# Performance work log

Hardware: AMD Instinct MI355X
Metric: run time of the kernel (lower is better)

## Reference

```python
import jax, jax.numpy as jnp
import numpy as np

IN_FEATURES = [32, 32]
OUT_FEATURES = [64, 64]
RANKS = [16, 16, 16, 16]


def _make_cores(key):
    dims = IN_FEATURES + OUT_FEATURES
    ranks = RANKS
    # init scale as in the torch module
    var = 2 ** (1.0 / len(dims)) / np.prod(np.power(np.array(ranks) + np.array(IN_FEATURES + IN_FEATURES), 1.0 / len(dims)))
    ub = float(np.sqrt(3.0 * var))
    ranks_ext = [ranks[-1]] + list(ranks)
    cores = []
    for i in range(len(dims)):
        key, k = jax.random.split(key)
        cores.append(jax.random.uniform(k, (ranks_ext[i], dims[i], ranks_ext[i + 1]), jnp.float32, -ub, ub))
    return cores, key


def setup_inputs() -> dict:
    key = jax.random.key(0)
    cores, key = _make_cores(key)
    key, kx, kb = jax.random.split(key, 3)
    x = jax.random.normal(kx, (8192, int(np.prod(IN_FEATURES))), jnp.float32)
    bias = jax.random.normal(kb, (int(np.prod(OUT_FEATURES)),), jnp.float32)
    return {"x": x, "core0": cores[0], "core1": cores[1], "core2": cores[2], "core3": cores[3], "bias": bias}


def reference(x, core0, core1, core2, core3, bias):
    # Tensor-ring contraction to build the dense weight, then linear.
    # core shapes: (16,32,16), (16,32,16), (16,64,16), (16,64,16)
    w = jnp.tensordot(core0, core1, axes=([2], [0]))        # (r, i0, i1, r)
    w = jnp.tensordot(w, core2, axes=([3], [0]))            # (r, i0, i1, o0, r)
    # last core: contract w's trailing rank with core axis 0 AND w's leading
    # rank with core's trailing rank (closes the ring) -> (i0, i1, o0, o1)
    w = jnp.tensordot(w, core3, axes=([4, 0], [0, 2]))
    d_out = int(np.prod(OUT_FEATURES))
    w = w.reshape(d_out, -1)                                # (4096, 1024)
    return x @ w.T + bias
```

## Files before the change

### kernel.cpp

```cpp
#include <hip/hip_runtime.h>
#include <hip/hip_bf16.h>
#include <stdint.h>

typedef unsigned short ushort_t;
typedef __attribute__((ext_vector_type(8))) short short8;
typedef __attribute__((ext_vector_type(4))) float floatx4;

__device__ __forceinline__ ushort_t f2bf(float f) {
    union { float f; unsigned u; } v; v.f = f;
    unsigned r = v.u + 0x7fffu + ((v.u >> 16) & 1u);
    return (ushort_t)(r >> 16);
}

__device__ __forceinline__ void async16(ushort_t* lds, const ushort_t* g) {
    __builtin_amdgcn_global_load_lds(
        (const __attribute__((address_space(1))) unsigned int*)g,
        (__attribute__((address_space(3))) unsigned int*)lds, 16, 0, 0);
}

__global__ __launch_bounds__(256) void prep_all(const float* __restrict__ x,
                                                const float* __restrict__ c0,
                                                const float* __restrict__ c1,
                                                const float* __restrict__ c2,
                                                const float* __restrict__ c3,
                                                ushort_t* __restrict__ Xb,
                                                ushort_t* __restrict__ A2b,
                                                ushort_t* __restrict__ Bg1) {
    const int b = blockIdx.x, t = threadIdx.x;
    if (b < 8192) {
        int i = b * 256 + t;
        float4 v = ((const float4*)x)[i];
        ushort4 r;
        r.x = f2bf(v.x); r.y = f2bf(v.y); r.z = f2bf(v.z); r.w = f2bf(v.w);
        ((ushort4*)Xb)[i] = r;
    } else if (b < 9216) {
        int id = (b - 8192) * 256 + t;
        int k = id & 255, ii = id >> 8;
        int r0 = k >> 4, r2 = k & 15;
        int i0 = ii >> 5, i1 = ii & 31;
        const float* p0 = c0 + (r0 * 32 + i0) * 16;
        const float* p1 = c1 + i1 * 16 + r2;
        float s = 0.f;
#pragma unroll
        for (int r1 = 0; r1 < 16; r1++) s += p0[r1] * p1[r1 * 512];
        A2b[id] = f2bf(s);
    } else {
        int id = (b - 9216) * 256 + t;
        int c = id & 1023, n = id >> 10;
        int bq = n >> 8, k = n & 255;
        int r0 = k >> 4, r2 = k & 15;
        int o0 = bq * 16 + (c >> 6), o1 = c & 63;
        const float* p2 = c2 + (r2 * 64 + o0) * 16;
        const float* p3 = c3 + o1 * 16 + r0;
        float s = 0.f;
#pragma unroll
        for (int r3 = 0; r3 < 16; r3++) s += p2[r3] * p3[r3 * 1024];
        Bg1[id] = f2bf(s);
    }
}

__global__ __launch_bounds__(256) void gemm1_u(const ushort_t* __restrict__ Xb,
                                               const ushort_t* __restrict__ Bg1,
                                               ushort_t* __restrict__ U) {
    __shared__ ushort_t As[128 * 32];
    __shared__ ushort_t Bs[128 * 32];
    const int t = threadIdx.x;
    const unsigned orig = blockIdx.x;
    const unsigned wg = (orig & 7) * 64 + (orig >> 3);
    const int row0 = (int)(wg >> 3) * 128;
    const int col0 = (int)(wg & 7) * 128;
    const int w = t >> 6, l = t & 63;
    const int wm = w >> 1, wn = w & 1;
    const int quad = l >> 4, ln = l & 15;

    floatx4 acc[4][4] = {};

    const ushort_t* aSrc = Xb  + (size_t)(row0 + (t >> 2)) * 1024 + (t & 3) * 8;
    const ushort_t* bSrc = Bg1 + (size_t)(col0 + (t >> 2)) * 1024 + (t & 3) * 8;

    for (int kk = 0; kk < 1024; kk += 32) {
        async16(&As[t * 8],        aSrc + kk);
        async16(&As[2048 + t * 8], aSrc + 64 * 1024 + kk);
        async16(&Bs[t * 8],        bSrc + kk);
        async16(&Bs[2048 + t * 8], bSrc + 64 * 1024 + kk);
        __syncthreads();

        short8 a[4], b[4];
#pragma unroll
        for (int ti = 0; ti < 4; ti++)
            a[ti] = *(const short8*)&As[(wm * 64 + ti * 16 + ln) * 32 + quad * 8];
#pragma unroll
        for (int tj = 0; tj < 4; tj++)
            b[tj] = *(const short8*)&Bs[(wn * 64 + tj * 16 + ln) * 32 + quad * 8];
#pragma unroll
        for (int ti = 0; ti < 4; ti++)
#pragma unroll
            for (int tj = 0; tj < 4; tj++)
                acc[ti][tj] = __builtin_amdgcn_mfma_f32_16x16x32_bf16(
                    a[ti], b[tj], acc[ti][tj], 0, 0, 0);
        __syncthreads();
    }

#pragma unroll
    for (int tj = 0; tj < 4; tj++) {
        const int n = col0 + wn * 64 + tj * 16 + ln;
#pragma unroll
        for (int ti = 0; ti < 4; ti++) {
            const int m = row0 + wm * 64 + ti * 16 + quad * 4;
#pragma unroll
            for (int r = 0; r < 4; r++)
                U[(size_t)(m + r) * 1024 + n] = f2bf(acc[ti][tj][r]);
        }
    }
}

__global__ __launch_bounds__(256) void gemm2_tr(const ushort_t* __restrict__ U,
                                                const ushort_t* __restrict__ A2b,
                                                const float* __restrict__ bias,
                                                float* __restrict__ out) {
    __shared__ ushort_t Us[4 * 128 * 32];
    __shared__ ushort_t A2s[32 * 264];
    const int t = threadIdx.x;
    const unsigned orig = blockIdx.x;
    const unsigned wg = (orig & 7) * 256 + (orig >> 3);
    const int jt = (int)(wg & 31), mt = (int)(wg >> 5);
    const int row0 = mt * 128;
    const int a0 = jt * 32;
    const int w = t >> 6, l = t & 63;
    const int wm = w >> 1, wn = w & 1;
    const int quad = l >> 4, ln = l & 15;

    {
        const int r = t >> 3, cb = t & 7;
#pragma unroll
        for (int s = 0; s < 4; s++) {
            int ch = cb + s * 8;
            short8 v = *(const short8*)&A2b[(size_t)(a0 + r) * 256 + ch * 8];
            *(short8*)&A2s[r * 264 + ch * 8] = v;
        }
    }

    floatx4 acc[4][4] = {};

    const ushort_t* uSrc = U + (size_t)(row0 + (t >> 2)) * 1024 + (t & 3) * 8;

    for (int kk = 0; kk < 256; kk += 32) {
#pragma unroll
        for (int b = 0; b < 4; b++) {
            async16(&Us[b * 4096 + t * 8],        uSrc + b * 256 + kk);
            async16(&Us[b * 4096 + 2048 + t * 8], uSrc + 64 * 1024 + b * 256 + kk);
        }
        __syncthreads();

        short8 bfrag = *(const short8*)&A2s[(wn * 16 + ln) * 264 + kk + quad * 8];
#pragma unroll
        for (int b = 0; b < 4; b++) {
            short8 au[4];
#pragma unroll
            for (int ti = 0; ti < 4; ti++)
                au[ti] = *(const short8*)&Us[b * 4096 + (wm * 64 + ti * 16 + ln) * 32 + quad * 8];
#pragma unroll
            for (int ti = 0; ti < 4; ti++)
                acc[b][ti] = __builtin_amdgcn_mfma_f32_16x16x32_bf16(
                    au[ti], bfrag, acc[b][ti], 0, 0, 0);
        }
        __syncthreads();
    }

    const int a = a0 + wn * 16 + ln;
    const float4 bv = ((const float4*)bias)[a];
#pragma unroll
    for (int ti = 0; ti < 4; ti++) {
        const int m = row0 + wm * 64 + ti * 16 + quad * 4;
#pragma unroll
        for (int r = 0; r < 4; r++) {
            float4 o;
            o.x = acc[0][ti][r] + bv.x;
            o.y = acc[1][ti][r] + bv.y;
            o.z = acc[2][ti][r] + bv.z;
            o.w = acc[3][ti][r] + bv.w;
            *(float4*)&out[(size_t)(m + r) * 4096 + (size_t)a * 4] = o;
        }
    }
}

extern "C" void kernel_launch(void* const* d_in, const int* in_sizes, int n_in,
                              void* d_out, int out_size, void* d_ws, size_t ws_size,
                              hipStream_t stream) {
    const float* x    = (const float*)d_in[0];
    const float* c0   = (const float*)d_in[1];
    const float* c1   = (const float*)d_in[2];
    const float* c2   = (const float*)d_in[3];
    const float* c3   = (const float*)d_in[4];
    const float* bias = (const float*)d_in[5];
    float* out = (float*)d_out;

    char* ws = (char*)d_ws;
    ushort_t* Xb  = (ushort_t*)out;
    ushort_t* U   = (ushort_t*)ws;
    ushort_t* A2b = (ushort_t*)(ws + (16u << 20));
    ushort_t* Bg1 = (ushort_t*)(ws + (17u << 20));

    hipLaunchKernelGGL(prep_all, dim3(13312), dim3(256), 0, stream,
                       x, c0, c1, c2, c3, Xb, A2b, Bg1);
    hipLaunchKernelGGL(gemm1_u, dim3(512), dim3(256), 0, stream, Xb, Bg1, U);
    hipLaunchKernelGGL(gemm2_tr, dim3(2048), dim3(256), 0, stream, U, A2b, bias, out);
}
```

Baseline: 256.5 us.

## Widen gemm2 tile to 64 A2 columns and keep A2 fragments in registers

```diff
diff --git a/kernel.cpp b/kernel.cpp
--- a/kernel.cpp
+++ b/kernel.cpp
@@ -119,32 +119,32 @@
                                                 const float* __restrict__ bias,
                                                 float* __restrict__ out) {
     __shared__ ushort_t Us[4 * 128 * 32];
-    __shared__ ushort_t A2s[32 * 264];
     const int t = threadIdx.x;
     const unsigned orig = blockIdx.x;
-    const unsigned wg = (orig & 7) * 256 + (orig >> 3);
-    const int jt = (int)(wg & 31), mt = (int)(wg >> 5);
+    const unsigned wg = (orig & 7) * 128 + (orig >> 3);
+    const int jt = (int)(wg & 15), mt = (int)(wg >> 4);
     const int row0 = mt * 128;
-    const int a0 = jt * 32;
+    const int a0 = jt * 64;
     const int w = t >> 6, l = t & 63;
     const int wm = w >> 1, wn = w & 1;
     const int quad = l >> 4, ln = l & 15;
 
-    {
-        const int r = t >> 3, cb = t & 7;
-#pragma unroll
-        for (int s = 0; s < 4; s++) {
-            int ch = cb + s * 8;
-            short8 v = *(const short8*)&A2b[(size_t)(a0 + r) * 256 + ch * 8];
-            *(short8*)&A2s[r * 264 + ch * 8] = v;
-        }
-    }
-
-    floatx4 acc[4][4] = {};
+    short8 a2f[2][8];
+#pragma unroll
+    for (int tj = 0; tj < 2; tj++) {
+        const ushort_t* ap = A2b + (size_t)(a0 + wn * 32 + tj * 16 + ln) * 256 + quad * 8;
+#pragma unroll
+        for (int s = 0; s < 8; s++)
+            a2f[tj][s] = *(const short8*)&ap[s * 32];
+    }
+
+    floatx4 acc[4][4][2] = {};
 
     const ushort_t* uSrc = U + (size_t)(row0 + (t >> 2)) * 1024 + (t & 3) * 8;
 
-    for (int kk = 0; kk < 256; kk += 32) {
+#pragma unroll
+    for (int kk8 = 0; kk8 < 8; kk8++) {
+        const int kk = kk8 * 32;
 #pragma unroll
         for (int b = 0; b < 4; b++) {
             async16(&Us[b * 4096 + t * 8],        uSrc + b * 256 + kk);
@@ -152,7 +152,6 @@
         }
         __syncthreads();
 
-        short8 bfrag = *(const short8*)&A2s[(wn * 16 + ln) * 264 + kk + quad * 8];
 #pragma unroll
         for (int b = 0; b < 4; b++) {
             short8 au[4];
@@ -161,25 +160,30 @@
                 au[ti] = *(const short8*)&Us[b * 4096 + (wm * 64 + ti * 16 + ln) * 32 + quad * 8];
 #pragma unroll
             for (int ti = 0; ti < 4; ti++)
-                acc[b][ti] = __builtin_amdgcn_mfma_f32_16x16x32_bf16(
-                    au[ti], bfrag, acc[b][ti], 0, 0, 0);
-        }
-        __syncthreads();
-    }
-
-    const int a = a0 + wn * 16 + ln;
-    const float4 bv = ((const float4*)bias)[a];
-#pragma unroll
-    for (int ti = 0; ti < 4; ti++) {
-        const int m = row0 + wm * 64 + ti * 16 + quad * 4;
-#pragma unroll
-        for (int r = 0; r < 4; r++) {
-            float4 o;
-            o.x = acc[0][ti][r] + bv.x;
-            o.y = acc[1][ti][r] + bv.y;
-            o.z = acc[2][ti][r] + bv.z;
-            o.w = acc[3][ti][r] + bv.w;
-            *(float4*)&out[(size_t)(m + r) * 4096 + (size_t)a * 4] = o;
+#pragma unroll
+                for (int tj = 0; tj < 2; tj++)
+                    acc[b][ti][tj] = __builtin_amdgcn_mfma_f32_16x16x32_bf16(
+                        au[ti], a2f[tj][kk8], acc[b][ti][tj], 0, 0, 0);
+        }
+        __syncthreads();
+    }
+
+#pragma unroll
+    for (int tj = 0; tj < 2; tj++) {
+        const int a = a0 + wn * 32 + tj * 16 + ln;
+        const float4 bv = ((const float4*)bias)[a];
+#pragma unroll
+        for (int ti = 0; ti < 4; ti++) {
+            const int m = row0 + wm * 64 + ti * 16 + quad * 4;
+#pragma unroll
+            for (int r = 0; r < 4; r++) {
+                float4 o;
+                o.x = acc[0][ti][tj][r] + bv.x;
+                o.y = acc[1][ti][tj][r] + bv.y;
+                o.z = acc[2][ti][tj][r] + bv.z;
+                o.w = acc[3][ti][tj][r] + bv.w;
+                *(float4*)&out[(size_t)(m + r) * 4096 + (size_t)a * 4] = o;
+            }
         }
     }
 }
@@ -204,5 +208,5 @@
     hipLaunchKernelGGL(prep_all, dim3(13312), dim3(256), 0, stream,
                        x, c0, c1, c2, c3, Xb, A2b, Bg1);
     hipLaunchKernelGGL(gemm1_u, dim3(512), dim3(256), 0, stream, Xb, Bg1, U);
-    hipLaunchKernelGGL(gemm2_tr, dim3(2048), dim3(256), 0, stream, U, A2b, bias, out);
-}
+    hipLaunchKernelGGL(gemm2_tr, dim3(1024), dim3(256), 0, stream, U, A2b, bias, out);
+}
```

Result: no change. 257.1 us (+0.2%).
